# Kernel tuning notes

Measured on AMD Instinct MI355X. Metric: run time of the kernel, lower is better.

## Reference

```python
import jax, jax.numpy as jnp
import numpy as np

B, T, I, H, O = 128, 512, 256, 512, 256


def setup_inputs() -> dict:
    key = jax.random.key(0)
    ks = jax.random.split(key, 20)
    s_i = 1.0 / np.sqrt(I)
    s_h = 1.0 / np.sqrt(H)
    inp = {
        "x": jax.random.normal(ks[0], (B, T, I), dtype=jnp.float32),
        "Wix_w": jax.random.normal(ks[1], (H, I), dtype=jnp.float32) * s_i,
        "Wix_b": jax.random.normal(ks[2], (H,), dtype=jnp.float32) * s_i,
        "Wih_w": jax.random.normal(ks[3], (H, H), dtype=jnp.float32) * s_h,
        "Wih_b": jax.random.normal(ks[4], (H,), dtype=jnp.float32) * s_h,
        "bi": jnp.zeros((H,), dtype=jnp.float32),
        "Wfx_w": jax.random.normal(ks[5], (H, I), dtype=jnp.float32) * s_i,
        "Wfx_b": jax.random.normal(ks[6], (H,), dtype=jnp.float32) * s_i,
        "Wfh_w": jax.random.normal(ks[7], (H, H), dtype=jnp.float32) * s_h,
        "Wfh_b": jax.random.normal(ks[8], (H,), dtype=jnp.float32) * s_h,
        "bf": jnp.zeros((H,), dtype=jnp.float32),
        "Wgx_w": jax.random.normal(ks[9], (H, I), dtype=jnp.float32) * s_i,
        "Wgx_b": jax.random.normal(ks[10], (H,), dtype=jnp.float32) * s_i,
        "Wgh_w": jax.random.normal(ks[11], (H, H), dtype=jnp.float32) * s_h,
        "Wgh_b": jax.random.normal(ks[12], (H,), dtype=jnp.float32) * s_h,
        "bg": jnp.zeros((H,), dtype=jnp.float32),
        "Wox_w": jax.random.normal(ks[13], (H, I), dtype=jnp.float32) * s_i,
        "Wox_b": jax.random.normal(ks[14], (H,), dtype=jnp.float32) * s_i,
        "Woh_w": jax.random.normal(ks[15], (H, H), dtype=jnp.float32) * s_h,
        "Woh_b": jax.random.normal(ks[16], (H,), dtype=jnp.float32) * s_h,
        "bo": jnp.zeros((H,), dtype=jnp.float32),
        "Wph_w": jax.random.normal(ks[17], (O, H), dtype=jnp.float32) * s_h,
        "Wph_b": jax.random.normal(ks[18], (O,), dtype=jnp.float32) * s_h,
        "bp": jnp.zeros((O,), dtype=jnp.float32),
    }
    return inp


def reference(x, Wix_w, Wix_b, Wih_w, Wih_b, bi,
              Wfx_w, Wfx_b, Wfh_w, Wfh_b, bf,
              Wgx_w, Wgx_b, Wgh_w, Wgh_b, bg,
              Wox_w, Wox_b, Woh_w, Woh_b, bo,
              Wph_w, Wph_b, bp):
    batch = x.shape[0]
    h0 = jnp.zeros((batch, Wih_w.shape[0]), dtype=x.dtype)
    c0 = jnp.zeros_like(h0)

    # Precompute all input projections across time in 4 big GEMMs
    # (same math as per-step Linear calls, just batched over t).
    ix = jnp.einsum('bti,hi->bth', x, Wix_w) + Wix_b + bi
    fx = jnp.einsum('bti,hi->bth', x, Wfx_w) + Wfx_b + bf
    gx = jnp.einsum('bti,hi->bth', x, Wgx_w) + Wgx_b + bg
    ox = jnp.einsum('bti,hi->bth', x, Wox_w) + Wox_b + bo

    def step(carry, xt):
        h, c = carry
        ixt, fxt, gxt, oxt = xt
        i = jax.nn.sigmoid(ixt + h @ Wih_w.T + Wih_b)
        f = jax.nn.sigmoid(fxt + h @ Wfh_w.T + Wfh_b)
        g = jnp.tanh(gxt + h @ Wgh_w.T + Wgh_b)
        o = jax.nn.sigmoid(oxt + h @ Woh_w.T + Woh_b)
        c_new = g * i + c * f
        h_new = jnp.tanh(c_new) * o
        p = h_new @ Wph_w.T + Wph_b + bp
        y = jax.nn.softmax(p, axis=1)
        return (h_new, c_new), y

    # scan over time: [T, B, H] layout
    xs = (jnp.swapaxes(ix, 0, 1), jnp.swapaxes(fx, 0, 1),
          jnp.swapaxes(gx, 0, 1), jnp.swapaxes(ox, 0, 1))
    _, ys = jax.lax.scan(step, (h0, c0), xs)
    return jnp.swapaxes(ys, 0, 1)  # [B, T, O]
```

## Files before the change

kernel.cpp:

```cpp
#include <hip/hip_runtime.h>
#include <hip/hip_bf16.h>
#include <math.h>

#define B_  128
#define T_  512
#define I_  256
#define H_  512
#define O_  256
#define NP  2048
#define BT  65536
#define HB  65536

struct PrepArgs {
    const float* Whw[4];
    const float* Wxw[4];
    const float* Wxb[4];
    const float* Whb[4];
    const float* bg[4];
    const float* Wph_w;
    const float* Wph_b;
    const float* bp;
    float* Wt; float* Wg; float* WgT; float* WphT;
    float* xb; float* hb; float* pb;
};

#define PREP_TOTAL (1048576 + 524288 + 524288 + 131072 + 2048 + 2048 + 256)

__global__ __launch_bounds__(256) void k_prep(PrepArgs a) {
    int idx = blockIdx.x * 256 + threadIdx.x;
    if (idx >= PREP_TOTAL) return;
    int q = idx;
    if (q < 1048576) {
        int k = q >> 11, n = q & 2047;
        int g = n & 3, h = n >> 2;
        a.Wt[q] = a.Whw[g][h * H_ + k];
        return;
    }
    q -= 1048576;
    if (q < 524288) {
        int n = q >> 8, i = q & 255;
        int g = n & 3, h = n >> 2;
        a.Wg[q] = a.Wxw[g][h * I_ + i];
        return;
    }
    q -= 524288;
    if (q < 524288) {
        int i = q >> 11, n = q & 2047;
        int g = n & 3, h = n >> 2;
        a.WgT[q] = a.Wxw[g][h * I_ + i];
        return;
    }
    q -= 524288;
    if (q < 131072) {
        int h = q >> 8, o = q & 255;
        a.WphT[q] = a.Wph_w[o * H_ + h];
        return;
    }
    q -= 131072;
    if (q < 2048) {
        int g = q & 3, h = q >> 2;
        a.xb[q] = a.Wxb[g][h] + a.bg[g][h];
        return;
    }
    q -= 2048;
    if (q < 2048) {
        int g = q & 3, h = q >> 2;
        a.hb[q] = a.Whb[g][h];
        return;
    }
    q -= 2048;
    a.pb[q] = a.Wph_b[q] + a.bp[q];
}

__global__ __launch_bounds__(256) void k_transpose(const float* __restrict__ x,
                                                   float* __restrict__ xT2) {
    __shared__ float lds[32][33];
    int tid = threadIdx.x;
    int tx = tid & 31, ty = tid >> 5;
    int j0 = blockIdx.x * 32;
    int i0 = blockIdx.y * 32;
    int t  = j0 >> 7;
    int b0 = j0 & 127;
#pragma unroll
    for (int rr = 0; rr < 4; ++rr) {
        int jj = ty + rr * 8;
        lds[jj][tx] = x[((size_t)(b0 + jj) * T_ + t) * I_ + i0 + tx];
    }
    __syncthreads();
#pragma unroll
    for (int rr = 0; rr < 4; ++rr) {
        int ii = ty + rr * 8;
        xT2[(size_t)(i0 + ii) * BT + j0 + tx] = lds[tx][ii];
    }
}

__global__ __launch_bounds__(256, 1) void k_xgemm(const float* __restrict__ A,
                                                  const float* __restrict__ Bm,
                                                  const float* __restrict__ bias,
                                                  float* __restrict__ C) {
    __shared__ float As[16][128];
    __shared__ float Bs[16][128];
    int tid = threadIdx.x;
    int tx = tid & 15, ty = tid >> 4;
    int m0 = blockIdx.y * 128, j0 = blockIdx.x * 128;
    float acc[8][8];
#pragma unroll
    for (int i = 0; i < 8; ++i)
#pragma unroll
        for (int j = 0; j < 8; ++j) acc[i][j] = 0.f;

    for (int kt = 0; kt < I_; kt += 16) {
#pragma unroll
        for (int pp = 0; pp < 2; ++pp) {
            int p = tid + pp * 256;
            int row = p >> 2, kq = (p & 3) << 2;
            float4 av = *(const float4*)&A[(size_t)(m0 + row) * I_ + kt + kq];
            As[kq + 0][row] = av.x; As[kq + 1][row] = av.y;
            As[kq + 2][row] = av.z; As[kq + 3][row] = av.w;
        }
#pragma unroll
        for (int pp = 0; pp < 2; ++pp) {
            int p = tid + pp * 256;
            int krow = p >> 5, c4 = (p & 31) << 2;
            *(float4*)&Bs[krow][c4] =
                *(const float4*)&Bm[(size_t)(kt + krow) * BT + j0 + c4];
        }
        __syncthreads();
#pragma unroll
        for (int k = 0; k < 16; ++k) {
            float a[8], b[8];
            *(float4*)&a[0] = *(const float4*)&As[k][ty * 4];
            *(float4*)&a[4] = *(const float4*)&As[k][64 + ty * 4];
            *(float4*)&b[0] = *(const float4*)&Bs[k][tx * 4];
            *(float4*)&b[4] = *(const float4*)&Bs[k][64 + tx * 4];
#pragma unroll
            for (int i = 0; i < 8; ++i)
#pragma unroll
                for (int j = 0; j < 8; ++j) acc[i][j] += a[i] * b[j];
        }
        __syncthreads();
    }
#pragma unroll
    for (int i = 0; i < 8; ++i) {
        int mrow = (i < 4) ? (ty * 4 + i) : (64 + ty * 4 + (i - 4));
        int m = m0 + mrow;
        float bv = bias[m];
        float4 v0 = {acc[i][0] + bv, acc[i][1] + bv, acc[i][2] + bv, acc[i][3] + bv};
        float4 v1 = {acc[i][4] + bv, acc[i][5] + bv, acc[i][6] + bv, acc[i][7] + bv};
        *(float4*)&C[(size_t)m * BT + j0 + tx * 4] = v0;
        *(float4*)&C[(size_t)m * BT + j0 + 64 + tx * 4] = v1;
    }
}

__device__ inline float sigm(float v) { return 1.f / (1.f + expf(-v)); }

template <bool USE_XP>
__global__ __launch_bounds__(256, 1) void k_step(const float* __restrict__ Wt,
                                                 const float* __restrict__ WgT,
                                                 const float* __restrict__ xp,
                                                 const float* __restrict__ xT2,
                                                 const float* __restrict__ xb,
                                                 const float* __restrict__ hb,
                                                 float* __restrict__ hist,
                                                 float* __restrict__ cT,
                                                 int t) {
    __shared__ float red[4][16][64];
    int tid = threadIdx.x;
    int wave = tid >> 6, lane = tid & 63;
    int nt = blockIdx.x >> 1, bh = blockIdx.x & 1;
    int n0 = nt * 16, b0 = bh * 64;
    int b = b0 + lane;

    const float* hrow = hist + (size_t)t * HB;
    float acc[16];
#pragma unroll
    for (int j = 0; j < 16; ++j) acc[j] = 0.f;

    {
        int k0 = wave * 128;
        const float* hp = hrow + (size_t)k0 * B_ + b;
        const float* wp = Wt + (size_t)k0 * NP + n0;
        float hv[8];
#pragma unroll
        for (int u = 0; u < 8; ++u) hv[u] = hp[u * B_];
        for (int kb = 0; kb < 128; kb += 8) {
            float hn[8];
            if (kb + 8 < 128) {
                const float* hp2 = hp + (size_t)(kb + 8) * B_;
#pragma unroll
                for (int u = 0; u < 8; ++u) hn[u] = hp2[u * B_];
            }
#pragma unroll
            for (int u = 0; u < 8; ++u) {
                const float* w = wp + (size_t)(kb + u) * NP;
                float h0 = hv[u];
#pragma unroll
                for (int j = 0; j < 4; ++j) {
                    float4 wv = *(const float4*)(w + j * 4);
                    acc[j * 4 + 0] += h0 * wv.x;
                    acc[j * 4 + 1] += h0 * wv.y;
                    acc[j * 4 + 2] += h0 * wv.z;
                    acc[j * 4 + 3] += h0 * wv.w;
                }
            }
#pragma unroll
            for (int u = 0; u < 8; ++u) hv[u] = hn[u];
        }
    }
    if (!USE_XP) {
        int i0 = wave * 64;
        const float* xpp = xT2 + (size_t)i0 * BT + (size_t)t * B_ + b;
        const float* wp  = WgT + (size_t)i0 * NP + n0;
#pragma unroll 4
        for (int ii = 0; ii < 64; ++ii) {
            float xv = xpp[(size_t)ii * BT];
            const float* w = wp + (size_t)ii * NP;
#pragma unroll
            for (int j = 0; j < 4; ++j) {
                float4 wv = *(const float4*)(w + j * 4);
                acc[j * 4 + 0] += xv * wv.x;
                acc[j * 4 + 1] += xv * wv.y;
                acc[j * 4 + 2] += xv * wv.z;
                acc[j * 4 + 3] += xv * wv.w;
            }
        }
    }
#pragma unroll
    for (int j = 0; j < 16; ++j) red[wave][j][lane] = acc[j];
    __syncthreads();

    int b_l = tid & 63, h_i = tid >> 6;
    int n = n0 + h_i * 4;
    int h = nt * 4 + h_i;
    int bb = b0 + b_l;
    float pre[4];
#pragma unroll
    for (int g = 0; g < 4; ++g) {
        int j = h_i * 4 + g;
        pre[g] = red[0][j][b_l] + red[1][j][b_l] + red[2][j][b_l] + red[3][j][b_l];
        pre[g] += hb[n + g];
        if (USE_XP)
            pre[g] += xp[(size_t)(n + g) * BT + (size_t)t * B_ + bb];
        else
            pre[g] += xb[n + g];
    }
    float iv = sigm(pre[0]);
    float fv = sigm(pre[1]);
    float gv = tanhf(pre[2]);
    float ov = sigm(pre[3]);
    float c  = cT[h * B_ + bb];
    float cn = gv * iv + c * fv;
    cT[h * B_ + bb] = cn;
    hist[(size_t)(t + 1) * HB + h * B_ + bb] = tanhf(cn) * ov;
}

__global__ __launch_bounds__(256, 1) void k_outproj(const float* __restrict__ WphT,
                                                    const float* __restrict__ pb,
                                                    const float* __restrict__ hist,
                                                    float* __restrict__ pT) {
    __shared__ float red[4][16][64];
    int tid = threadIdx.x;
    int wave = tid >> 6, lane = tid & 63;
    int t = blockIdx.y;
    int ot = blockIdx.x >> 1, bh = blockIdx.x & 1;
    int o0 = ot * 16, b0 = bh * 64;
    int b = b0 + lane;

    const float* hrow = hist + (size_t)(t + 1) * HB;
    float acc[16];
#pragma unroll
    for (int j = 0; j < 16; ++j) acc[j] = 0.f;

    int k0 = wave * 128;
    const float* hp = hrow + (size_t)k0 * B_ + b;
    const float* wp = WphT + (size_t)k0 * O_ + o0;
    float hv[8];
#pragma unroll
    for (int u = 0; u < 8; ++u) hv[u] = hp[u * B_];
    for (int kb = 0; kb < 128; kb += 8) {
        float hn[8];
        if (kb + 8 < 128) {
            const float* hp2 = hp + (size_t)(kb + 8) * B_;
#pragma unroll
            for (int u = 0; u < 8; ++u) hn[u] = hp2[u * B_];
        }
#pragma unroll
        for (int u = 0; u < 8; ++u) {
            const float* w = wp + (size_t)(kb + u) * O_;
            float h0 = hv[u];
#pragma unroll
            for (int j = 0; j < 4; ++j) {
                float4 wv = *(const float4*)(w + j * 4);
                acc[j * 4 + 0] += h0 * wv.x;
                acc[j * 4 + 1] += h0 * wv.y;
                acc[j * 4 + 2] += h0 * wv.z;
                acc[j * 4 + 3] += h0 * wv.w;
            }
        }
#pragma unroll
        for (int u = 0; u < 8; ++u) hv[u] = hn[u];
    }
#pragma unroll
    for (int j = 0; j < 16; ++j) red[wave][j][lane] = acc[j];
    __syncthreads();

    int b_l = tid & 63, oi = tid >> 6;
    int bb = b0 + b_l;
#pragma unroll
    for (int g = 0; g < 4; ++g) {
        int j = oi * 4 + g;
        int o = o0 + j;
        float v = red[0][j][b_l] + red[1][j][b_l] + red[2][j][b_l] + red[3][j][b_l] + pb[o];
        pT[(size_t)t * (O_ * B_) + (size_t)o * B_ + bb] = v;
    }
}

__global__ __launch_bounds__(256, 1) void k_softmax(const float* __restrict__ pT,
                                                    float* __restrict__ out) {
    __shared__ float sm[32][257];
    __shared__ float rmax[32][8];
    __shared__ float rsum[32][8];
    int tid = threadIdx.x;
    int t = blockIdx.x >> 2, bq = blockIdx.x & 3;
    int b0 = bq * 32;
    const float* src = pT + (size_t)t * (O_ * B_);

#pragma unroll 4
    for (int it = 0; it < 32; ++it) {
        int idx = it * 256 + tid;
        int o = idx >> 5, b_l = idx & 31;
        sm[b_l][o] = src[(size_t)o * B_ + b0 + b_l];
    }
    __syncthreads();

    int b_l = tid >> 3, oc = tid & 7;
    float m = -3.4e38f;
#pragma unroll 4
    for (int oo = 0; oo < 32; ++oo) m = fmaxf(m, sm[b_l][oc * 32 + oo]);
    rmax[b_l][oc] = m;
    __syncthreads();
    float mm = rmax[b_l][0];
#pragma unroll
    for (int c = 1; c < 8; ++c) mm = fmaxf(mm, rmax[b_l][c]);

    float s = 0.f;
#pragma unroll 4
    for (int oo = 0; oo < 32; ++oo) s += expf(sm[b_l][oc * 32 + oo] - mm);
    rsum[b_l][oc] = s;
    __syncthreads();
    float st = 0.f;
#pragma unroll
    for (int c = 0; c < 8; ++c) st += rsum[b_l][c];
    float inv = 1.f / st;

    int bb = b0 + b_l;
    float* dst = out + ((size_t)bb * T_ + t) * O_ + oc * 32;
#pragma unroll 4
    for (int oo = 0; oo < 32; ++oo)
        dst[oo] = expf(sm[b_l][oc * 32 + oo] - mm) * inv;
}

extern "C" void kernel_launch(void* const* d_in, const int* in_sizes, int n_in,
                              void* d_out, int out_size, void* d_ws, size_t ws_size,
                              hipStream_t stream) {
    const float* x = (const float*)d_in[0];

    float* ws = (float*)d_ws;
    size_t off = 0;
    auto alloc = [&](size_t n) { float* p = ws + off; off += n; return p; };

    float* hist = alloc((size_t)513 * HB);
    float* cT   = alloc(HB);
    float* Wt   = alloc((size_t)512 * NP);
    float* Wg   = alloc((size_t)NP * I_);
    float* WgT  = alloc((size_t)I_ * NP);
    float* WphT = alloc((size_t)H_ * O_);
    float* xb   = alloc(NP);
    float* hb   = alloc(NP);
    float* pb   = alloc(O_);
    float* xT2  = alloc((size_t)I_ * BT);
    size_t baseBytes = off * sizeof(float);
    size_t xpBytes   = (size_t)NP * BT * sizeof(float);

    bool useXp = (ws_size >= baseBytes + xpBytes);
    float* xp = ws + off;
    float* pT = xT2;

    if (ws_size < baseBytes) return;

    hipMemsetAsync(hist, 0, HB * sizeof(float), stream);
    hipMemsetAsync(cT, 0, HB * sizeof(float), stream);

    PrepArgs pa;
    for (int g = 0; g < 4; ++g) {
        pa.Wxw[g] = (const float*)d_in[1 + 5 * g];
        pa.Wxb[g] = (const float*)d_in[2 + 5 * g];
        pa.Whw[g] = (const float*)d_in[3 + 5 * g];
        pa.Whb[g] = (const float*)d_in[4 + 5 * g];
        pa.bg[g]  = (const float*)d_in[5 + 5 * g];
    }
    pa.Wph_w = (const float*)d_in[21];
    pa.Wph_b = (const float*)d_in[22];
    pa.bp    = (const float*)d_in[23];
    pa.Wt = Wt; pa.Wg = Wg; pa.WgT = WgT; pa.WphT = WphT;
    pa.xb = xb; pa.hb = hb; pa.pb = pb;

    k_prep<<<(PREP_TOTAL + 255) / 256, 256, 0, stream>>>(pa);
    k_transpose<<<dim3(BT / 32, I_ / 32), 256, 0, stream>>>(x, xT2);

    if (useXp)
        k_xgemm<<<dim3(BT / 128, NP / 128), 256, 0, stream>>>(Wg, xT2, xb, xp);

    for (int t = 0; t < T_; ++t) {
        if (useXp)
            k_step<true><<<256, 256, 0, stream>>>(Wt, WgT, xp, xT2, xb, hb, hist, cT, t);
        else
            k_step<false><<<256, 256, 0, stream>>>(Wt, WgT, xp, xT2, xb, hb, hist, cT, t);
    }

    k_outproj<<<dim3(32, T_), 256, 0, stream>>>(WphT, pb, hist, pT);
    k_softmax<<<T_ * 4, 256, 0, stream>>>(pT, (float*)d_out);
}
```

Baseline: 16.98 ms.

## Fuse LSTM time loop into persistent cooperative kernel with LDS-resident weights

Replaces the 512 per-timestep kernel launches with one persistent cooperative kernel that uses grid.sync between steps. Each block keeps its slice of the recurrent and input weights in shared memory and holds the cell state in registers. The input projection is now computed inside the recurrence instead of by a precomputed x-GEMM. This removes launch overhead and the repeated global weight reads, but puts input-projection FLOPs on the serial critical path and relies on grid-wide barriers across 256 co-resident blocks.

```diff
diff --git a/kernel.cpp b/kernel.cpp
--- a/kernel.cpp
+++ b/kernel.cpp
@@ -1,6 +1,8 @@
 #include <hip/hip_runtime.h>
-#include <hip/hip_bf16.h>
+#include <hip/hip_cooperative_groups.h>
 #include <math.h>
+
+namespace cg = cooperative_groups;
 
 #define B_  128
 #define T_  512
@@ -20,11 +22,11 @@
     const float* Wph_w;
     const float* Wph_b;
     const float* bp;
-    float* Wt; float* Wg; float* WgT; float* WphT;
+    float* Wt; float* WgT; float* WphT;
     float* xb; float* hb; float* pb;
 };
 
-#define PREP_TOTAL (1048576 + 524288 + 524288 + 131072 + 2048 + 2048 + 256)
+#define PREP_TOTAL (1048576 + 524288 + 131072 + 2048 + 2048 + 256)
 
 __global__ __launch_bounds__(256) void k_prep(PrepArgs a) {
     int idx = blockIdx.x * 256 + threadIdx.x;
@@ -37,13 +39,6 @@
         return;
     }
     q -= 1048576;
-    if (q < 524288) {
-        int n = q >> 8, i = q & 255;
-        int g = n & 3, h = n >> 2;
-        a.Wg[q] = a.Wxw[g][h * I_ + i];
-        return;
-    }
-    q -= 524288;
     if (q < 524288) {
         int i = q >> 11, n = q & 2047;
         int g = n & 3, h = n >> 2;
@@ -94,164 +89,133 @@
     }
 }
 
-__global__ __launch_bounds__(256, 1) void k_xgemm(const float* __restrict__ A,
-                                                  const float* __restrict__ Bm,
-                                                  const float* __restrict__ bias,
-                                                  float* __restrict__ C) {
-    __shared__ float As[16][128];
-    __shared__ float Bs[16][128];
-    int tid = threadIdx.x;
-    int tx = tid & 15, ty = tid >> 4;
-    int m0 = blockIdx.y * 128, j0 = blockIdx.x * 128;
-    float acc[8][8];
-#pragma unroll
-    for (int i = 0; i < 8; ++i)
-#pragma unroll
-        for (int j = 0; j < 8; ++j) acc[i][j] = 0.f;
-
-    for (int kt = 0; kt < I_; kt += 16) {
-#pragma unroll
-        for (int pp = 0; pp < 2; ++pp) {
-            int p = tid + pp * 256;
-            int row = p >> 2, kq = (p & 3) << 2;
-            float4 av = *(const float4*)&A[(size_t)(m0 + row) * I_ + kt + kq];
-            As[kq + 0][row] = av.x; As[kq + 1][row] = av.y;
-            As[kq + 2][row] = av.z; As[kq + 3][row] = av.w;
-        }
-#pragma unroll
-        for (int pp = 0; pp < 2; ++pp) {
-            int p = tid + pp * 256;
-            int krow = p >> 5, c4 = (p & 31) << 2;
-            *(float4*)&Bs[krow][c4] =
-                *(const float4*)&Bm[(size_t)(kt + krow) * BT + j0 + c4];
-        }
-        __syncthreads();
-#pragma unroll
-        for (int k = 0; k < 16; ++k) {
-            float a[8], b[8];
-            *(float4*)&a[0] = *(const float4*)&As[k][ty * 4];
-            *(float4*)&a[4] = *(const float4*)&As[k][64 + ty * 4];
-            *(float4*)&b[0] = *(const float4*)&Bs[k][tx * 4];
-            *(float4*)&b[4] = *(const float4*)&Bs[k][64 + tx * 4];
-#pragma unroll
-            for (int i = 0; i < 8; ++i)
-#pragma unroll
-                for (int j = 0; j < 8; ++j) acc[i][j] += a[i] * b[j];
-        }
-        __syncthreads();
-    }
-#pragma unroll
-    for (int i = 0; i < 8; ++i) {
-        int mrow = (i < 4) ? (ty * 4 + i) : (64 + ty * 4 + (i - 4));
-        int m = m0 + mrow;
-        float bv = bias[m];
-        float4 v0 = {acc[i][0] + bv, acc[i][1] + bv, acc[i][2] + bv, acc[i][3] + bv};
-        float4 v1 = {acc[i][4] + bv, acc[i][5] + bv, acc[i][6] + bv, acc[i][7] + bv};
-        *(float4*)&C[(size_t)m * BT + j0 + tx * 4] = v0;
-        *(float4*)&C[(size_t)m * BT + j0 + 64 + tx * 4] = v1;
-    }
-}
-
 __device__ inline float sigm(float v) { return 1.f / (1.f + expf(-v)); }
 
-template <bool USE_XP>
-__global__ __launch_bounds__(256, 1) void k_step(const float* __restrict__ Wt,
+__global__ __launch_bounds__(256, 1) void k_scan(const float* __restrict__ Wt,
                                                  const float* __restrict__ WgT,
-                                                 const float* __restrict__ xp,
                                                  const float* __restrict__ xT2,
                                                  const float* __restrict__ xb,
                                                  const float* __restrict__ hb,
-                                                 float* __restrict__ hist,
-                                                 float* __restrict__ cT,
-                                                 int t) {
+                                                 float* __restrict__ hist) {
+    __shared__ float Wl[512 * 16];
+    __shared__ float Xl[256 * 16];
     __shared__ float red[4][16][64];
+    cg::grid_group grid = cg::this_grid();
+
     int tid = threadIdx.x;
     int wave = tid >> 6, lane = tid & 63;
     int nt = blockIdx.x >> 1, bh = blockIdx.x & 1;
     int n0 = nt * 16, b0 = bh * 64;
     int b = b0 + lane;
 
-    const float* hrow = hist + (size_t)t * HB;
-    float acc[16];
-#pragma unroll
-    for (int j = 0; j < 16; ++j) acc[j] = 0.f;
-
-    {
-        int k0 = wave * 128;
-        const float* hp = hrow + (size_t)k0 * B_ + b;
-        const float* wp = Wt + (size_t)k0 * NP + n0;
-        float hv[8];
-#pragma unroll
-        for (int u = 0; u < 8; ++u) hv[u] = hp[u * B_];
-        for (int kb = 0; kb < 128; kb += 8) {
-            float hn[8];
-            if (kb + 8 < 128) {
-                const float* hp2 = hp + (size_t)(kb + 8) * B_;
-#pragma unroll
-                for (int u = 0; u < 8; ++u) hn[u] = hp2[u * B_];
+    for (int idx = tid; idx < 512 * 4; idx += 256) {
+        int k = idx >> 2, j4 = (idx & 3) << 2;
+        *(float4*)&Wl[k * 16 + j4] = *(const float4*)&Wt[(size_t)k * NP + n0 + j4];
+    }
+    for (int idx = tid; idx < 256 * 4; idx += 256) {
+        int i = idx >> 2, j4 = (idx & 3) << 2;
+        *(float4*)&Xl[i * 16 + j4] = *(const float4*)&WgT[(size_t)i * NP + n0 + j4];
+    }
+
+    int b_l = tid & 63, h_i = tid >> 6;
+    int n_e = n0 + h_i * 4;
+    int h_e = nt * 4 + h_i;
+    int bb = b0 + b_l;
+    float xb4[4], hb4[4];
+#pragma unroll
+    for (int g = 0; g < 4; ++g) { xb4[g] = xb[n_e + g]; hb4[g] = hb[n_e + g]; }
+    float c_reg = 0.f;
+
+    __syncthreads();
+
+    for (int t = 0; t < T_; ++t) {
+        const float* hrow = hist + (size_t)t * HB;
+        float acc[16];
+#pragma unroll
+        for (int j = 0; j < 16; ++j) acc[j] = 0.f;
+
+        {
+            int k0 = wave * 128;
+            const float* hp = hrow + (size_t)k0 * B_ + b;
+            const float* wl = &Wl[k0 * 16];
+            float hv[8];
+#pragma unroll
+            for (int u = 0; u < 8; ++u) hv[u] = hp[u * B_];
+            for (int kb = 0; kb < 128; kb += 8) {
+                float hn[8];
+                if (kb + 8 < 128) {
+                    const float* hp2 = hp + (size_t)(kb + 8) * B_;
+#pragma unroll
+                    for (int u = 0; u < 8; ++u) hn[u] = hp2[u * B_];
+                }
+#pragma unroll
+                for (int u = 0; u < 8; ++u) {
+                    const float* w = wl + (kb + u) * 16;
+                    float h0 = hv[u];
+#pragma unroll
+                    for (int j = 0; j < 4; ++j) {
+                        float4 wv = *(const float4*)(w + j * 4);
+                        acc[j * 4 + 0] += h0 * wv.x;
+                        acc[j * 4 + 1] += h0 * wv.y;
+                        acc[j * 4 + 2] += h0 * wv.z;
+                        acc[j * 4 + 3] += h0 * wv.w;
+                    }
+                }
+#pragma unroll
+                for (int u = 0; u < 8; ++u) hv[u] = hn[u];
             }
-#pragma unroll
-            for (int u = 0; u < 8; ++u) {
-                const float* w = wp + (size_t)(kb + u) * NP;
-                float h0 = hv[u];
-#pragma unroll
-                for (int j = 0; j < 4; ++j) {
-                    float4 wv = *(const float4*)(w + j * 4);
-                    acc[j * 4 + 0] += h0 * wv.x;
-                    acc[j * 4 + 1] += h0 * wv.y;
-                    acc[j * 4 + 2] += h0 * wv.z;
-                    acc[j * 4 + 3] += h0 * wv.w;
+        }
+        {
+            int i0 = wave * 64;
+            const float* xpp = xT2 + (size_t)i0 * BT + (size_t)t * B_ + b;
+            float xv[8];
+#pragma unroll
+            for (int u = 0; u < 8; ++u) xv[u] = xpp[(size_t)u * BT];
+            for (int ib = 0; ib < 64; ib += 8) {
+                float xn[8];
+                if (ib + 8 < 64) {
+                    const float* xp2 = xpp + (size_t)(ib + 8) * BT;
+#pragma unroll
+                    for (int u = 0; u < 8; ++u) xn[u] = xp2[(size_t)u * BT];
                 }
+#pragma unroll
+                for (int u = 0; u < 8; ++u) {
+                    const float* w = &Xl[(i0 + ib + u) * 16];
+                    float x0 = xv[u];
+#pragma unroll
+                    for (int j = 0; j < 4; ++j) {
+                        float4 wv = *(const float4*)(w + j * 4);
+                        acc[j * 4 + 0] += x0 * wv.x;
+                        acc[j * 4 + 1] += x0 * wv.y;
+                        acc[j * 4 + 2] += x0 * wv.z;
+                        acc[j * 4 + 3] += x0 * wv.w;
+                    }
+                }
+#pragma unroll
+                for (int u = 0; u < 8; ++u) xv[u] = xn[u];
             }
-#pragma unroll
-            for (int u = 0; u < 8; ++u) hv[u] = hn[u];
-        }
-    }
-    if (!USE_XP) {
-        int i0 = wave * 64;
-        const float* xpp = xT2 + (size_t)i0 * BT + (size_t)t * B_ + b;
-        const float* wp  = WgT + (size_t)i0 * NP + n0;
-#pragma unroll 4
-        for (int ii = 0; ii < 64; ++ii) {
-            float xv = xpp[(size_t)ii * BT];
-            const float* w = wp + (size_t)ii * NP;
-#pragma unroll
-            for (int j = 0; j < 4; ++j) {
-                float4 wv = *(const float4*)(w + j * 4);
-                acc[j * 4 + 0] += xv * wv.x;
-                acc[j * 4 + 1] += xv * wv.y;
-                acc[j * 4 + 2] += xv * wv.z;
-                acc[j * 4 + 3] += xv * wv.w;
-            }
-        }
-    }
-#pragma unroll
-    for (int j = 0; j < 16; ++j) red[wave][j][lane] = acc[j];
-    __syncthreads();
-
-    int b_l = tid & 63, h_i = tid >> 6;
-    int n = n0 + h_i * 4;
-    int h = nt * 4 + h_i;
-    int bb = b0 + b_l;
-    float pre[4];
-#pragma unroll
-    for (int g = 0; g < 4; ++g) {
-        int j = h_i * 4 + g;
-        pre[g] = red[0][j][b_l] + red[1][j][b_l] + red[2][j][b_l] + red[3][j][b_l];
-        pre[g] += hb[n + g];
-        if (USE_XP)
-            pre[g] += xp[(size_t)(n + g) * BT + (size_t)t * B_ + bb];
-        else
-            pre[g] += xb[n + g];
-    }
-    float iv = sigm(pre[0]);
-    float fv = sigm(pre[1]);
-    float gv = tanhf(pre[2]);
-    float ov = sigm(pre[3]);
-    float c  = cT[h * B_ + bb];
-    float cn = gv * iv + c * fv;
-    cT[h * B_ + bb] = cn;
-    hist[(size_t)(t + 1) * HB + h * B_ + bb] = tanhf(cn) * ov;
+        }
+#pragma unroll
+        for (int j = 0; j < 16; ++j) red[wave][j][lane] = acc[j];
+        __syncthreads();
+
+        float pre[4];
+#pragma unroll
+        for (int g = 0; g < 4; ++g) {
+            int j = h_i * 4 + g;
+            pre[g] = red[0][j][b_l] + red[1][j][b_l] + red[2][j][b_l] + red[3][j][b_l]
+                   + hb4[g] + xb4[g];
+        }
+        float iv = sigm(pre[0]);
+        float fv = sigm(pre[1]);
+        float gv = tanhf(pre[2]);
+        float ov = sigm(pre[3]);
+        float cn = gv * iv + c_reg * fv;
+        c_reg = cn;
+        hist[(size_t)(t + 1) * HB + h_e * B_ + bb] = tanhf(cn) * ov;
+
+        grid.sync();
+    }
 }
 
 __global__ __launch_bounds__(256, 1) void k_outproj(const float* __restrict__ WphT,
@@ -370,26 +334,18 @@
     auto alloc = [&](size_t n) { float* p = ws + off; off += n; return p; };
 
     float* hist = alloc((size_t)513 * HB);
-    float* cT   = alloc(HB);
     float* Wt   = alloc((size_t)512 * NP);
-    float* Wg   = alloc((size_t)NP * I_);
     float* WgT  = alloc((size_t)I_ * NP);
     float* WphT = alloc((size_t)H_ * O_);
     float* xb   = alloc(NP);
     float* hb   = alloc(NP);
     float* pb   = alloc(O_);
     float* xT2  = alloc((size_t)I_ * BT);
-    size_t baseBytes = off * sizeof(float);
-    size_t xpBytes   = (size_t)NP * BT * sizeof(float);
-
-    bool useXp = (ws_size >= baseBytes + xpBytes);
-    float* xp = ws + off;
-    float* pT = xT2;
-
-    if (ws_size < baseBytes) return;
+    float* pT   = xT2;
+
+    if (ws_size < off * sizeof(float)) return;
 
     hipMemsetAsync(hist, 0, HB * sizeof(float), stream);
-    hipMemsetAsync(cT, 0, HB * sizeof(float), stream);
 
     PrepArgs pa;
     for (int g = 0; g < 4; ++g) {
@@ -402,20 +358,17 @@
     pa.Wph_w = (const float*)d_in[21];
     pa.Wph_b = (const float*)d_in[22];
     pa.bp    = (const float*)d_in[23];
-    pa.Wt = Wt; pa.Wg = Wg; pa.WgT = WgT; pa.WphT = WphT;
+    pa.Wt = Wt; pa.WgT = WgT; pa.WphT = WphT;
     pa.xb = xb; pa.hb = hb; pa.pb = pb;
 
     k_prep<<<(PREP_TOTAL + 255) / 256, 256, 0, stream>>>(pa);
     k_transpose<<<dim3(BT / 32, I_ / 32), 256, 0, stream>>>(x, xT2);
 
-    if (useXp)
-        k_xgemm<<<dim3(BT / 128, NP / 128), 256, 0, stream>>>(Wg, xT2, xb, xp);
-
-    for (int t = 0; t < T_; ++t) {
-        if (useXp)
-            k_step<true><<<256, 256, 0, stream>>>(Wt, WgT, xp, xT2, xb, hb, hist, cT, t);
-        else
-            k_step<false><<<256, 256, 0, stream>>>(Wt, WgT, xp, xT2, xb, hb, hist, cT, t);
+    {
+        void* args[] = {(void*)&Wt, (void*)&WgT, (void*)&xT2,
+                        (void*)&xb, (void*)&hb, (void*)&hist};
+        hipLaunchCooperativeKernel((const void*)k_scan, dim3(256), dim3(256),
+                                   args, 0, stream);
     }
 
     k_outproj<<<dim3(32, T_), 256, 0, stream>>>(WphT, pb, hist, pT);
```

New measurement: 21.81 ms. 1.28x slower.
